# Kernel optimization log

Measured on AMD Instinct MI355X. Metric: run time of the kernel, lower is better.

Reference implementation:

```python
import jax, jax.numpy as jnp
import numpy as np

N_NODES = 100_000
N_EDGES = 1_600_000
HEADS = 3
DIMS = [6, 8, 16, 32]  # in -> conv1 -> conv2 -> conv3 out_feats


def _edge_gat(x, ef, src, dst, W, We, al, ar, ae, b, n_nodes):
    """DGL EdgeGATConv: edge feats modulate attention logits; messages are alpha * W h_src."""
    H, D = al.shape
    ft = (x @ W.T).reshape(n_nodes, H, D)          # [N,H,D] projected node feats
    fe = (ef @ We.T).reshape(-1, H, D)             # [E,H,D] projected edge feats
    el = jnp.sum(ft * al, axis=-1)                 # [N,H]
    er = jnp.sum(ft * ar, axis=-1)                 # [N,H]
    ee = jnp.sum(fe * ae, axis=-1)                 # [E,H]
    e = jax.nn.leaky_relu(el[src] + er[dst] + ee, 0.2)  # [E,H] (DGL default slope 0.2)
    # segment softmax over incoming edges of each dst node
    m = jax.ops.segment_max(e, dst, num_segments=n_nodes)
    m = jnp.where(jnp.isfinite(m), m, 0.0)         # zero-in-degree nodes
    ex = jnp.exp(e - m[dst])
    denom = jax.ops.segment_sum(ex, dst, num_segments=n_nodes)
    a = ex / jnp.maximum(denom[dst], 1e-9)         # [E,H]
    msg = a[:, :, None] * ft[src]                  # [E,H,D]
    out = jax.ops.segment_sum(msg, dst, num_segments=n_nodes)  # [N,H,D]
    return out + b.reshape(1, H, D)


def setup_inputs() -> dict:
    key = jax.random.key(0)
    ks = jax.random.split(key, 32)
    d = {
        "node_feats": jax.random.normal(ks[0], (N_NODES, DIMS[0]), jnp.float32),
        "edge_feats": jax.random.uniform(ks[1], (N_EDGES, 1), jnp.float32),
        "src": jax.random.randint(ks[2], (N_EDGES,), 0, N_NODES, jnp.int32),
        "dst": jax.random.randint(ks[3], (N_EDGES,), 0, N_NODES, jnp.int32),
    }
    ki = 4
    for i in range(3):
        fin, fout = DIMS[i], DIMS[i + 1]
        s = 1.0 / np.sqrt(fin)
        d[f"W{i+1}"] = jax.random.normal(ks[ki], (HEADS * fout, fin), jnp.float32) * s; ki += 1
        d[f"We{i+1}"] = jax.random.normal(ks[ki], (HEADS * fout, 1), jnp.float32); ki += 1
        d[f"al{i+1}"] = jax.random.normal(ks[ki], (HEADS, fout), jnp.float32) * 0.1; ki += 1
        d[f"ar{i+1}"] = jax.random.normal(ks[ki], (HEADS, fout), jnp.float32) * 0.1; ki += 1
        d[f"ae{i+1}"] = jax.random.normal(ks[ki], (HEADS, fout), jnp.float32) * 0.1; ki += 1
        d[f"b{i+1}"] = jnp.zeros((HEADS * fout,), jnp.float32)
    for name, (fo, fi) in [("l1", (16, 32)), ("l2", (4, 16)), ("l3", (1, 4)), ("l4", (1, HEADS))]:
        s = 1.0 / np.sqrt(fi)
        d[name + "w"] = jax.random.uniform(ks[ki], (fo, fi), jnp.float32, -s, s); ki += 1
        d[name + "b"] = jax.random.uniform(ks[ki], (fo,), jnp.float32, -s, s); ki += 1
    return d


def reference(node_feats, edge_feats, src, dst,
              W1, We1, al1, ar1, ae1, b1,
              W2, We2, al2, ar2, ae2, b2,
              W3, We3, al3, ar3, ae3, b3,
              l1w, l1b, l2w, l2b, l3w, l3b, l4w, l4b):
    n = node_feats.shape[0]
    h1 = _edge_gat(node_feats, edge_feats, src, dst, W1, We1, al1, ar1, ae1, b1, n)  # [N,3,8]
    h2 = _edge_gat(h1.mean(axis=1), edge_feats, src, dst, W2, We2, al2, ar2, ae2, b2, n)  # [N,3,16]
    h3 = _edge_gat(h2.mean(axis=1), edge_feats, src, dst, W3, We3, al3, ar3, ae3, b3, n)  # [N,3,32]
    # per-(node,head) MLP head: 32 -> 16 -> 4 -> 1
    x = jax.nn.leaky_relu(h3 @ l1w.T + l1b, 0.01)
    x = jax.nn.leaky_relu(x @ l2w.T + l2b, 0.01)
    x = x @ l3w.T + l3b                            # [N,3,1]
    feats = x.reshape(n, -1) @ l4w.T + l4b         # [N,1] combine heads
    return jnp.max(feats, axis=0)                  # [1]
```

## Files before the change

### kernel.cpp

```cpp
#include <hip/hip_runtime.h>
#include <hip/hip_bf16.h>
#include <hip/hip_fp16.h>

#define HEADS 3

union HU { uint4 u; __half2 h[4]; };

__global__ void prep_ce_kernel(const float* __restrict__ We1, const float* __restrict__ ae1,
                               const float* __restrict__ We2, const float* __restrict__ ae2,
                               const float* __restrict__ We3, const float* __restrict__ ae3,
                               float* __restrict__ ce) {
    int t = threadIdx.x;
    if (t >= 9) return;
    int l = t / 3, h = t % 3;
    const float* We = (l == 0) ? We1 : (l == 1) ? We2 : We3;
    const float* ae = (l == 0) ? ae1 : (l == 1) ? ae2 : ae3;
    int D = (l == 0) ? 8 : (l == 1) ? 16 : 32;
    float s = 0.f;
    for (int d = 0; d < D; d++) s += We[h * D + d] * ae[h * D + d];
    ce[t] = s;
}

__global__ void hist_kernel(const int* __restrict__ dst, int* __restrict__ deg, int E) {
    int tid = blockIdx.x * blockDim.x + threadIdx.x;
    if (tid < E) atomicAdd(&deg[dst[tid]], 1);
}

#define SCAN_BLK 1024
__global__ void scan1_kernel(const int* __restrict__ deg, int* __restrict__ row_ptr,
                             int* __restrict__ partials, int N) {
    __shared__ int sm[SCAN_BLK];
    int t = threadIdx.x;
    int g = blockIdx.x * SCAN_BLK + t;
    int v = (g < N) ? deg[g] : 0;
    sm[t] = v;
    __syncthreads();
    for (int off = 1; off < SCAN_BLK; off <<= 1) {
        int x = (t >= off) ? sm[t - off] : 0;
        __syncthreads();
        sm[t] += x;
        __syncthreads();
    }
    if (g < N) row_ptr[g] = sm[t] - v;
    if (t == SCAN_BLK - 1) partials[blockIdx.x] = sm[t];
}

__global__ void scan2_kernel(int* __restrict__ partials, int NB) {
    __shared__ int sm[128];
    int t = threadIdx.x;
    int v = (t < NB) ? partials[t] : 0;
    sm[t] = v;
    __syncthreads();
    for (int off = 1; off < 128; off <<= 1) {
        int x = (t >= off) ? sm[t - off] : 0;
        __syncthreads();
        sm[t] += x;
        __syncthreads();
    }
    if (t < NB) partials[t] = sm[t] - v;
    if (t == 127) partials[NB] = sm[127];
}

__global__ void scan3_kernel(int* __restrict__ row_ptr, const int* __restrict__ partials,
                             int N, int NB) {
    int g = blockIdx.x * SCAN_BLK + threadIdx.x;
    if (g < N) row_ptr[g] += partials[blockIdx.x];
    if (blockIdx.x == 0 && threadIdx.x == 0) row_ptr[N] = partials[NB];
}

__global__ void scatter_kernel(const int* __restrict__ src, const int* __restrict__ dst,
                               const float* __restrict__ ef, const int* __restrict__ row_ptr,
                               int* __restrict__ cnt, int2* __restrict__ erec, int E) {
    int tid = blockIdx.x * blockDim.x + threadIdx.x;
    if (tid >= E) return;
    int d = dst[tid];
    int pos = row_ptr[d] + atomicAdd(&cnt[d], 1);
    int2 r;
    r.x = src[tid];
    r.y = __float_as_int(ef[tid]);
    erec[pos] = r;
}

template <int FIN, int D, bool MEAN_PREV>
__launch_bounds__(256)
__global__ void node_kernel(const float* __restrict__ xin,
                            const float* __restrict__ W,
                            const float* __restrict__ al,
                            const float* __restrict__ ar,
                            __half* __restrict__ ft,
                            float* __restrict__ el, float* __restrict__ er,
                            int N) {
    int tid = blockIdx.x * blockDim.x + threadIdx.x;
    if (tid >= N * HEADS) return;
    int n = tid / HEADS, h = tid % HEADS;
    float x[FIN];
    if (MEAN_PREV) {
        #pragma unroll
        for (int k = 0; k < FIN; k++)
            x[k] = (xin[(n * HEADS + 0) * FIN + k] +
                    xin[(n * HEADS + 1) * FIN + k] +
                    xin[(n * HEADS + 2) * FIN + k]) * (1.0f / 3.0f);
    } else {
        #pragma unroll
        for (int k = 0; k < FIN; k++) x[k] = xin[n * FIN + k];
    }
    float fv[D];
    float e_l = 0.f, e_r = 0.f;
    #pragma unroll
    for (int d = 0; d < D; d++) {
        const float* wr = &W[(h * D + d) * FIN];
        float f = 0.f;
        #pragma unroll
        for (int k = 0; k < FIN; k++) f += x[k] * wr[k];
        fv[d] = f;
        e_l += f * al[h * D + d];
        e_r += f * ar[h * D + d];
    }
    uint4* dst16 = (uint4*)(ft + (size_t)tid * D);
    #pragma unroll
    for (int q = 0; q < D / 8; q++) {
        HU u;
        #pragma unroll
        for (int j = 0; j < 4; j++)
            u.h[j] = __floats2half2_rn(fv[q * 8 + 2 * j], fv[q * 8 + 2 * j + 1]);
        dst16[q] = u.u;
    }
    el[tid] = e_l;
    er[tid] = e_r;
}

template <int D>
__launch_bounds__(256)
__global__ void agg_kernel(const int* __restrict__ row_ptr, const int2* __restrict__ erec,
                           const __half* __restrict__ ft,
                           const float* __restrict__ el, const float* __restrict__ er,
                           const float* __restrict__ ce,
                           const float* __restrict__ b,
                           float* __restrict__ out,
                           int N) {
    int w = threadIdx.x >> 6;
    int l = threadIdx.x & 63;
    int wl = l / 6;
    int rem = l - wl * 6;
    int s = rem >= 3 ? 1 : 0;
    int h = rem - s * 3;
    int n = (blockIdx.x * 4 + w) * 10 + wl;
    bool active = (wl < 10) && (n < N);

    float m = -3.0e38f, ssum = 0.f;
    float msg[D];
    #pragma unroll
    for (int d = 0; d < D; d++) msg[d] = 0.f;
    int unit = n * HEADS + h;
    float ceh = ce[h];

    if (active) {
        int beg = row_ptr[n], end = row_ptr[n + 1];
        int cnt = end - beg;
        int half = (cnt + 1) >> 1;
        int es = beg + s * half;
        int ee = s ? end : (beg + half);
        float ern = er[unit];

        int e = es;
        for (; e + 3 < ee; e += 4) {
            int2 r0 = erec[e + 0], r1 = erec[e + 1], r2 = erec[e + 2], r3 = erec[e + 3];
            float v0 = el[r0.x * HEADS + h] + ern + __int_as_float(r0.y) * ceh;
            float v1 = el[r1.x * HEADS + h] + ern + __int_as_float(r1.y) * ceh;
            float v2 = el[r2.x * HEADS + h] + ern + __int_as_float(r2.y) * ceh;
            float v3 = el[r3.x * HEADS + h] + ern + __int_as_float(r3.y) * ceh;
            v0 = v0 > 0.f ? v0 : 0.2f * v0;
            v1 = v1 > 0.f ? v1 : 0.2f * v1;
            v2 = v2 > 0.f ? v2 : 0.2f * v2;
            v3 = v3 > 0.f ? v3 : 0.2f * v3;
            float cm = fmaxf(fmaxf(v0, v1), fmaxf(v2, v3));
            if (cm > m) {
                float sc = __expf(m - cm);
                ssum *= sc;
                #pragma unroll
                for (int d = 0; d < D; d++) msg[d] *= sc;
                m = cm;
            }
            float x0 = __expf(v0 - m), x1 = __expf(v1 - m);
            float x2 = __expf(v2 - m), x3 = __expf(v3 - m);
            ssum += (x0 + x1) + (x2 + x3);
            const uint4* f0 = (const uint4*)(ft + ((size_t)r0.x * HEADS + h) * D);
            const uint4* f1 = (const uint4*)(ft + ((size_t)r1.x * HEADS + h) * D);
            const uint4* f2 = (const uint4*)(ft + ((size_t)r2.x * HEADS + h) * D);
            const uint4* f3 = (const uint4*)(ft + ((size_t)r3.x * HEADS + h) * D);
            #pragma unroll
            for (int q = 0; q < D / 8; q++) {
                HU a0, a1, a2, a3;
                a0.u = f0[q]; a1.u = f1[q]; a2.u = f2[q]; a3.u = f3[q];
                #pragma unroll
                for (int j = 0; j < 4; j++) {
                    float2 p0 = __half22float2(a0.h[j]);
                    float2 p1 = __half22float2(a1.h[j]);
                    float2 p2 = __half22float2(a2.h[j]);
                    float2 p3 = __half22float2(a3.h[j]);
                    msg[q * 8 + 2 * j + 0] += x0 * p0.x + x1 * p1.x + x2 * p2.x + x3 * p3.x;
                    msg[q * 8 + 2 * j + 1] += x0 * p0.y + x1 * p1.y + x2 * p2.y + x3 * p3.y;
                }
            }
        }
        for (; e < ee; e++) {
            int2 r = erec[e];
            float v = el[r.x * HEADS + h] + ern + __int_as_float(r.y) * ceh;
            v = v > 0.f ? v : 0.2f * v;
            if (v > m) {
                float sc = __expf(m - v);
                ssum *= sc;
                #pragma unroll
                for (int d = 0; d < D; d++) msg[d] *= sc;
                m = v;
            }
            float x = __expf(v - m);
            ssum += x;
            const uint4* fr = (const uint4*)(ft + ((size_t)r.x * HEADS + h) * D);
            #pragma unroll
            for (int q = 0; q < D / 8; q++) {
                HU a; a.u = fr[q];
                #pragma unroll
                for (int j = 0; j < 4; j++) {
                    float2 p = __half22float2(a.h[j]);
                    msg[q * 8 + 2 * j + 0] += x * p.x;
                    msg[q * 8 + 2 * j + 1] += x * p.y;
                }
            }
        }
    }

    int pl = (s ? (l - 3) : (l + 3)) & 63;
    float om = __shfl(m, pl);
    float osum = __shfl(ssum, pl);
    float M = fmaxf(m, om);
    float sA = __expf(m - M);
    float sB = __expf(om - M);
    float tot = ssum * sA + osum * sB;
    float inv = 1.0f / fmaxf(tot, 1e-9f);
    #pragma unroll
    for (int d = 0; d < D; d++)
        msg[d] = msg[d] * sA + __shfl(msg[d], pl) * sB;

    if (active) {
        int lo = s * (D / 2);
        float* ob = out + (size_t)unit * D + lo;
        #pragma unroll
        for (int d = 0; d < D / 2; d += 4) {
            float4 v;
            v.x = msg[lo + d + 0] * inv + b[h * D + lo + d + 0];
            v.y = msg[lo + d + 1] * inv + b[h * D + lo + d + 1];
            v.z = msg[lo + d + 2] * inv + b[h * D + lo + d + 2];
            v.w = msg[lo + d + 3] * inv + b[h * D + lo + d + 3];
            *(float4*)(ob + d) = v;
        }
    }
}

__global__ void mlp_max_kernel(const float* __restrict__ h3,
                               const float* __restrict__ l1w, const float* __restrict__ l1b,
                               const float* __restrict__ l2w, const float* __restrict__ l2b,
                               const float* __restrict__ l3w, const float* __restrict__ l3b,
                               const float* __restrict__ l4w, const float* __restrict__ l4b,
                               unsigned int* __restrict__ maxkey, int N) {
    int tid = blockIdx.x * blockDim.x + threadIdx.x;
    float feat = -3.0e38f;
    if (tid < N) {
        float acc = l4b[0];
        #pragma unroll
        for (int h = 0; h < HEADS; h++) {
            const float4* vp = (const float4*)&h3[((size_t)tid * HEADS + h) * 32];
            float v[32];
            #pragma unroll
            for (int q = 0; q < 8; q++) {
                float4 t = vp[q];
                v[q * 4 + 0] = t.x; v[q * 4 + 1] = t.y; v[q * 4 + 2] = t.z; v[q * 4 + 3] = t.w;
            }
            float y1[16];
            #pragma unroll
            for (int i = 0; i < 16; i++) {
                float s = l1b[i];
                const float* w = &l1w[i * 32];
                #pragma unroll
                for (int k = 0; k < 32; k++) s += v[k] * w[k];
                y1[i] = s > 0.f ? s : 0.01f * s;
            }
            float y2[4];
            #pragma unroll
            for (int i = 0; i < 4; i++) {
                float s = l2b[i];
                const float* w = &l2w[i * 16];
                #pragma unroll
                for (int k = 0; k < 16; k++) s += y1[k] * w[k];
                y2[i] = s > 0.f ? s : 0.01f * s;
            }
            float y3 = l3b[0];
            #pragma unroll
            for (int k = 0; k < 4; k++) y3 += y2[k] * l3w[k];
            acc += y3 * l4w[h];
        }
        feat = acc;
    }
    #pragma unroll
    for (int off = 32; off > 0; off >>= 1)
        feat = fmaxf(feat, __shfl_down(feat, off));
    if ((threadIdx.x & 63) == 0) {
        unsigned int u = __float_as_uint(feat);
        unsigned int key = (u & 0x80000000u) ? ~u : (u | 0x80000000u);
        atomicMax(maxkey, key);
    }
}

__global__ void finalize_kernel(const unsigned int* __restrict__ maxkey, float* __restrict__ out) {
    unsigned int key = *maxkey;
    unsigned int u = (key & 0x80000000u) ? (key & 0x7FFFFFFFu) : ~key;
    out[0] = __uint_as_float(u);
}

extern "C" void kernel_launch(void* const* d_in, const int* in_sizes, int n_in,
                              void* d_out, int out_size, void* d_ws, size_t ws_size,
                              hipStream_t stream) {
    const float* node_feats = (const float*)d_in[0];
    const float* edge_feats = (const float*)d_in[1];
    const int* src = (const int*)d_in[2];
    const int* dst = (const int*)d_in[3];
    const float* W1  = (const float*)d_in[4];
    const float* We1 = (const float*)d_in[5];
    const float* al1 = (const float*)d_in[6];
    const float* ar1 = (const float*)d_in[7];
    const float* ae1 = (const float*)d_in[8];
    const float* b1  = (const float*)d_in[9];
    const float* W2  = (const float*)d_in[10];
    const float* We2 = (const float*)d_in[11];
    const float* al2 = (const float*)d_in[12];
    const float* ar2 = (const float*)d_in[13];
    const float* ae2 = (const float*)d_in[14];
    const float* b2  = (const float*)d_in[15];
    const float* W3  = (const float*)d_in[16];
    const float* We3 = (const float*)d_in[17];
    const float* al3 = (const float*)d_in[18];
    const float* ar3 = (const float*)d_in[19];
    const float* ae3 = (const float*)d_in[20];
    const float* b3  = (const float*)d_in[21];
    const float* l1w = (const float*)d_in[22];
    const float* l1b = (const float*)d_in[23];
    const float* l2w = (const float*)d_in[24];
    const float* l2b = (const float*)d_in[25];
    const float* l3w = (const float*)d_in[26];
    const float* l3b = (const float*)d_in[27];
    const float* l4w = (const float*)d_in[28];
    const float* l4b = (const float*)d_in[29];

    const int N = in_sizes[0] / 6;
    const int E = in_sizes[2];
    const int NB = (N + SCAN_BLK - 1) / SCAN_BLK;

    char* ws = (char*)d_ws;
    size_t off = 0;
    auto alloc = [&](size_t bytes) -> void* {
        void* p = ws + off;
        off = (off + bytes + 255) & ~(size_t)255;
        return p;
    };
    int* deg            = (int*)alloc((size_t)N * 4);
    int* cnt            = (int*)alloc((size_t)N * 4);
    unsigned int* mkey  = (unsigned int*)alloc(4);
    size_t zero_bytes   = off;
    int* row_ptr        = (int*)alloc((size_t)(N + 1) * 4);
    int* partials       = (int*)alloc((size_t)(NB + 1) * 4);
    int2* erec          = (int2*)alloc((size_t)E * 8);
    __half* ft          = (__half*)alloc((size_t)N * 96 * 2);
    float* outb         = (float*)alloc((size_t)N * 96 * 4);
    float* el           = (float*)alloc((size_t)N * 3 * 4);
    float* er           = (float*)alloc((size_t)N * 3 * 4);
    float* ce           = (float*)alloc(9 * 4);

    hipMemsetAsync(d_ws, 0, zero_bytes, stream);

    prep_ce_kernel<<<1, 16, 0, stream>>>(We1, ae1, We2, ae2, We3, ae3, ce);
    hist_kernel<<<(E + 255) / 256, 256, 0, stream>>>(dst, deg, E);
    scan1_kernel<<<NB, SCAN_BLK, 0, stream>>>(deg, row_ptr, partials, N);
    scan2_kernel<<<1, 128, 0, stream>>>(partials, NB);
    scan3_kernel<<<NB, SCAN_BLK, 0, stream>>>(row_ptr, partials, N, NB);
    scatter_kernel<<<(E + 255) / 256, 256, 0, stream>>>(src, dst, edge_feats, row_ptr, cnt,
                                                        erec, E);

    const int NH = N * HEADS;
    const int gb = (NH + 255) / 256;
    const int gb_agg = (N + 39) / 40;

    node_kernel<6, 8, false><<<gb, 256, 0, stream>>>(node_feats, W1, al1, ar1, ft, el, er, N);
    agg_kernel<8><<<gb_agg, 256, 0, stream>>>(row_ptr, erec, ft, el, er, ce + 0, b1, outb, N);
    node_kernel<8, 16, true><<<gb, 256, 0, stream>>>(outb, W2, al2, ar2, ft, el, er, N);
    agg_kernel<16><<<gb_agg, 256, 0, stream>>>(row_ptr, erec, ft, el, er, ce + 3, b2, outb, N);
    node_kernel<16, 32, true><<<gb, 256, 0, stream>>>(outb, W3, al3, ar3, ft, el, er, N);
    agg_kernel<32><<<gb_agg, 256, 0, stream>>>(row_ptr, erec, ft, el, er, ce + 6, b3, outb, N);

    mlp_max_kernel<<<(N + 255) / 256, 256, 0, stream>>>(outb, l1w, l1b, l2w, l2b, l3w, l3b,
                                                        l4w, l4b, mkey, N);
    finalize_kernel<<<1, 1, 0, stream>>>(mkey, (float*)d_out);
}
```

Before: 520.9 us.

## Build CSR via source-sorted intermediate so per-destination edges are ordered by source

```diff
diff --git a/kernel.cpp b/kernel.cpp
--- a/kernel.cpp
+++ b/kernel.cpp
@@ -21,9 +21,13 @@
     ce[t] = s;
 }
 
-__global__ void hist_kernel(const int* __restrict__ dst, int* __restrict__ deg, int E) {
+__global__ void hist2_kernel(const int* __restrict__ src, const int* __restrict__ dst,
+                             int* __restrict__ sdeg, int* __restrict__ ddeg, int E) {
     int tid = blockIdx.x * blockDim.x + threadIdx.x;
-    if (tid < E) atomicAdd(&deg[dst[tid]], 1);
+    if (tid < E) {
+        atomicAdd(&sdeg[src[tid]], 1);
+        atomicAdd(&ddeg[dst[tid]], 1);
+    }
 }
 
 #define SCAN_BLK 1024
@@ -68,17 +72,23 @@
     if (blockIdx.x == 0 && threadIdx.x == 0) row_ptr[N] = partials[NB];
 }
 
-__global__ void scatter_kernel(const int* __restrict__ src, const int* __restrict__ dst,
-                               const float* __restrict__ ef, const int* __restrict__ row_ptr,
-                               int* __restrict__ cnt, int2* __restrict__ erec, int E) {
+__global__ void scatter_src_kernel(const int* __restrict__ src, const int* __restrict__ dst,
+                                   const float* __restrict__ ef, const int* __restrict__ srow,
+                                   int* __restrict__ scnt, int4* __restrict__ sedge, int E) {
     int tid = blockIdx.x * blockDim.x + threadIdx.x;
     if (tid >= E) return;
-    int d = dst[tid];
-    int pos = row_ptr[d] + atomicAdd(&cnt[d], 1);
-    int2 r;
-    r.x = src[tid];
-    r.y = __float_as_int(ef[tid]);
-    erec[pos] = r;
+    int s = src[tid];
+    int pos = srow[s] + atomicAdd(&scnt[s], 1);
+    sedge[pos] = make_int4(s, dst[tid], __float_as_int(ef[tid]), 0);
+}
+
+__global__ void scatter_dst_kernel(const int4* __restrict__ sedge, const int* __restrict__ drow,
+                                   int* __restrict__ dcnt, int2* __restrict__ erec, int E) {
+    int tid = blockIdx.x * blockDim.x + threadIdx.x;
+    if (tid >= E) return;
+    int4 q = sedge[tid];
+    int pos = drow[q.y] + atomicAdd(&dcnt[q.y], 1);
+    erec[pos] = make_int2(q.x, q.z);
 }
 
 template <int FIN, int D, bool MEAN_PREV>
@@ -156,15 +166,11 @@
 
     if (active) {
         int beg = row_ptr[n], end = row_ptr[n + 1];
-        int cnt = end - beg;
-        int half = (cnt + 1) >> 1;
-        int es = beg + s * half;
-        int ee = s ? end : (beg + half);
         float ern = er[unit];
 
-        int e = es;
-        for (; e + 3 < ee; e += 4) {
-            int2 r0 = erec[e + 0], r1 = erec[e + 1], r2 = erec[e + 2], r3 = erec[e + 3];
+        int e = beg + s;
+        for (; e + 6 < end; e += 8) {
+            int2 r0 = erec[e + 0], r1 = erec[e + 2], r2 = erec[e + 4], r3 = erec[e + 6];
             float v0 = el[r0.x * HEADS + h] + ern + __int_as_float(r0.y) * ceh;
             float v1 = el[r1.x * HEADS + h] + ern + __int_as_float(r1.y) * ceh;
             float v2 = el[r2.x * HEADS + h] + ern + __int_as_float(r2.y) * ceh;
@@ -203,7 +209,7 @@
                 }
             }
         }
-        for (; e < ee; e++) {
+        for (; e < end; e += 2) {
             int2 r = erec[e];
             float v = el[r.x * HEADS + h] + ern + __int_as_float(r.y) * ceh;
             v = v > 0.f ? v : 0.2f * v;
@@ -362,12 +368,16 @@
         off = (off + bytes + 255) & ~(size_t)255;
         return p;
     };
-    int* deg            = (int*)alloc((size_t)N * 4);
-    int* cnt            = (int*)alloc((size_t)N * 4);
+    int* sdeg           = (int*)alloc((size_t)N * 4);
+    int* ddeg           = (int*)alloc((size_t)N * 4);
+    int* scnt           = (int*)alloc((size_t)N * 4);
+    int* dcnt           = (int*)alloc((size_t)N * 4);
     unsigned int* mkey  = (unsigned int*)alloc(4);
     size_t zero_bytes   = off;
-    int* row_ptr        = (int*)alloc((size_t)(N + 1) * 4);
+    int* srow           = (int*)alloc((size_t)(N + 1) * 4);
+    int* drow           = (int*)alloc((size_t)(N + 1) * 4);
     int* partials       = (int*)alloc((size_t)(NB + 1) * 4);
+    int4* sedge         = (int4*)alloc((size_t)E * 16);
     int2* erec          = (int2*)alloc((size_t)E * 8);
     __half* ft          = (__half*)alloc((size_t)N * 96 * 2);
     float* outb         = (float*)alloc((size_t)N * 96 * 4);
@@ -378,23 +388,27 @@
     hipMemsetAsync(d_ws, 0, zero_bytes, stream);
 
     prep_ce_kernel<<<1, 16, 0, stream>>>(We1, ae1, We2, ae2, We3, ae3, ce);
-    hist_kernel<<<(E + 255) / 256, 256, 0, stream>>>(dst, deg, E);
-    scan1_kernel<<<NB, SCAN_BLK, 0, stream>>>(deg, row_ptr, partials, N);
+    hist2_kernel<<<(E + 255) / 256, 256, 0, stream>>>(src, dst, sdeg, ddeg, E);
+    scan1_kernel<<<NB, SCAN_BLK, 0, stream>>>(ddeg, drow, partials, N);
     scan2_kernel<<<1, 128, 0, stream>>>(partials, NB);
-    scan3_kernel<<<NB, SCAN_BLK, 0, stream>>>(row_ptr, partials, N, NB);
-    scatter_kernel<<<(E + 255) / 256, 256, 0, stream>>>(src, dst, edge_feats, row_ptr, cnt,
-                                                        erec, E);
+    scan3_kernel<<<NB, SCAN_BLK, 0, stream>>>(drow, partials, N, NB);
+    scan1_kernel<<<NB, SCAN_BLK, 0, stream>>>(sdeg, srow, partials, N);
+    scan2_kernel<<<1, 128, 0, stream>>>(partials, NB);
+    scan3_kernel<<<NB, SCAN_BLK, 0, stream>>>(srow, partials, N, NB);
+    scatter_src_kernel<<<(E + 255) / 256, 256, 0, stream>>>(src, dst, edge_feats, srow, scnt,
+                                                            sedge, E);
+    scatter_dst_kernel<<<(E + 255) / 256, 256, 0, stream>>>(sedge, drow, dcnt, erec, E);
 
     const int NH = N * HEADS;
     const int gb = (NH + 255) / 256;
     const int gb_agg = (N + 39) / 40;
 
     node_kernel<6, 8, false><<<gb, 256, 0, stream>>>(node_feats, W1, al1, ar1, ft, el, er, N);
-    agg_kernel<8><<<gb_agg, 256, 0, stream>>>(row_ptr, erec, ft, el, er, ce + 0, b1, outb, N);
+    agg_kernel<8><<<gb_agg, 256, 0, stream>>>(drow, erec, ft, el, er, ce + 0, b1, outb, N);
     node_kernel<8, 16, true><<<gb, 256, 0, stream>>>(outb, W2, al2, ar2, ft, el, er, N);
-    agg_kernel<16><<<gb_agg, 256, 0, stream>>>(row_ptr, erec, ft, el, er, ce + 3, b2, outb, N);
+    agg_kernel<16><<<gb_agg, 256, 0, stream>>>(drow, erec, ft, el, er, ce + 3, b2, outb, N);
     node_kernel<16, 32, true><<<gb, 256, 0, stream>>>(outb, W3, al3, ar3, ft, el, er, N);
-    agg_kernel<32><<<gb_agg, 256, 0, stream>>>(row_ptr, erec, ft, el, er, ce + 6, b3, outb, N);
+    agg_kernel<32><<<gb_agg, 256, 0, stream>>>(drow, erec, ft, el, er, ce + 6, b3, outb, N);
 
     mlp_max_kernel<<<(N + 255) / 256, 256, 0, stream>>>(outb, l1w, l1b, l2w, l2b, l3w, l3b,
                                                         l4w, l4b, mkey, N);
```

Measured after the change: 663.1 us. 1.27x slower.

## Sort nodes by degree for balanced aggregation and reuse histogram ranks in scatter

Applied to the files above, without the earlier changes.

```diff
diff --git a/kernel.cpp b/kernel.cpp
--- a/kernel.cpp
+++ b/kernel.cpp
@@ -21,9 +21,10 @@
     ce[t] = s;
 }
 
-__global__ void hist_kernel(const int* __restrict__ dst, int* __restrict__ deg, int E) {
+__global__ void hist_rank_kernel(const int* __restrict__ dst, int* __restrict__ deg,
+                                 int* __restrict__ rank, int E) {
     int tid = blockIdx.x * blockDim.x + threadIdx.x;
-    if (tid < E) atomicAdd(&deg[dst[tid]], 1);
+    if (tid < E) rank[tid] = atomicAdd(&deg[dst[tid]], 1);
 }
 
 #define SCAN_BLK 1024
@@ -70,15 +71,35 @@
 
 __global__ void scatter_kernel(const int* __restrict__ src, const int* __restrict__ dst,
                                const float* __restrict__ ef, const int* __restrict__ row_ptr,
-                               int* __restrict__ cnt, int2* __restrict__ erec, int E) {
+                               const int* __restrict__ rank, int2* __restrict__ erec, int E) {
     int tid = blockIdx.x * blockDim.x + threadIdx.x;
     if (tid >= E) return;
     int d = dst[tid];
-    int pos = row_ptr[d] + atomicAdd(&cnt[d], 1);
+    int pos = row_ptr[d] + rank[tid];
     int2 r;
     r.x = src[tid];
     r.y = __float_as_int(ef[tid]);
     erec[pos] = r;
+}
+
+__global__ void degbin_hist_kernel(const int* __restrict__ deg, int* __restrict__ bins, int N) {
+    int n = blockIdx.x * blockDim.x + threadIdx.x;
+    if (n < N) atomicAdd(&bins[min(deg[n], 63)], 1);
+}
+
+__global__ void degbin_scan_kernel(const int* __restrict__ bins, int* __restrict__ bscan) {
+    if (threadIdx.x == 0) {
+        int run = 0;
+        for (int i = 0; i < 64; i++) { bscan[i] = run; run += bins[i]; }
+    }
+}
+
+__global__ void degbin_scatter_kernel(const int* __restrict__ deg, const int* __restrict__ bscan,
+                                      int* __restrict__ bcnt, int* __restrict__ order, int N) {
+    int n = blockIdx.x * blockDim.x + threadIdx.x;
+    if (n >= N) return;
+    int bin = min(deg[n], 63);
+    order[bscan[bin] + atomicAdd(&bcnt[bin], 1)] = n;
 }
 
 template <int FIN, int D, bool MEAN_PREV>
@@ -132,6 +153,7 @@
 template <int D>
 __launch_bounds__(256)
 __global__ void agg_kernel(const int* __restrict__ row_ptr, const int2* __restrict__ erec,
+                           const int* __restrict__ order,
                            const __half* __restrict__ ft,
                            const float* __restrict__ el, const float* __restrict__ er,
                            const float* __restrict__ ce,
@@ -144,8 +166,10 @@
     int rem = l - wl * 6;
     int s = rem >= 3 ? 1 : 0;
     int h = rem - s * 3;
-    int n = (blockIdx.x * 4 + w) * 10 + wl;
-    bool active = (wl < 10) && (n < N);
+    int slot = (blockIdx.x * 4 + w) * 10 + wl;
+    bool active = (wl < 10) && (slot < N);
+    int n = active ? order[slot] : 0;
+    int blane = l - h;
 
     float m = -3.0e38f, ssum = 0.f;
     float msg[D];
@@ -164,7 +188,15 @@
 
         int e = es;
         for (; e + 3 < ee; e += 4) {
-            int2 r0 = erec[e + 0], r1 = erec[e + 1], r2 = erec[e + 2], r3 = erec[e + 3];
+            int2 r0 = make_int2(0, 0), r1 = r0, r2 = r0, r3 = r0;
+            if (h == 0) {
+                r0 = erec[e + 0]; r1 = erec[e + 1];
+                r2 = erec[e + 2]; r3 = erec[e + 3];
+            }
+            r0.x = __shfl(r0.x, blane); r0.y = __shfl(r0.y, blane);
+            r1.x = __shfl(r1.x, blane); r1.y = __shfl(r1.y, blane);
+            r2.x = __shfl(r2.x, blane); r2.y = __shfl(r2.y, blane);
+            r3.x = __shfl(r3.x, blane); r3.y = __shfl(r3.y, blane);
             float v0 = el[r0.x * HEADS + h] + ern + __int_as_float(r0.y) * ceh;
             float v1 = el[r1.x * HEADS + h] + ern + __int_as_float(r1.y) * ceh;
             float v2 = el[r2.x * HEADS + h] + ern + __int_as_float(r2.y) * ceh;
@@ -363,9 +395,13 @@
         return p;
     };
     int* deg            = (int*)alloc((size_t)N * 4);
-    int* cnt            = (int*)alloc((size_t)N * 4);
+    int* bins           = (int*)alloc(64 * 4);
+    int* bcnt           = (int*)alloc(64 * 4);
     unsigned int* mkey  = (unsigned int*)alloc(4);
     size_t zero_bytes   = off;
+    int* bscan          = (int*)alloc(64 * 4);
+    int* order          = (int*)alloc((size_t)N * 4);
+    int* rank           = (int*)alloc((size_t)E * 4);
     int* row_ptr        = (int*)alloc((size_t)(N + 1) * 4);
     int* partials       = (int*)alloc((size_t)(NB + 1) * 4);
     int2* erec          = (int2*)alloc((size_t)E * 8);
@@ -378,23 +414,26 @@
     hipMemsetAsync(d_ws, 0, zero_bytes, stream);
 
     prep_ce_kernel<<<1, 16, 0, stream>>>(We1, ae1, We2, ae2, We3, ae3, ce);
-    hist_kernel<<<(E + 255) / 256, 256, 0, stream>>>(dst, deg, E);
+    hist_rank_kernel<<<(E + 255) / 256, 256, 0, stream>>>(dst, deg, rank, E);
     scan1_kernel<<<NB, SCAN_BLK, 0, stream>>>(deg, row_ptr, partials, N);
     scan2_kernel<<<1, 128, 0, stream>>>(partials, NB);
     scan3_kernel<<<NB, SCAN_BLK, 0, stream>>>(row_ptr, partials, N, NB);
-    scatter_kernel<<<(E + 255) / 256, 256, 0, stream>>>(src, dst, edge_feats, row_ptr, cnt,
+    scatter_kernel<<<(E + 255) / 256, 256, 0, stream>>>(src, dst, edge_feats, row_ptr, rank,
                                                         erec, E);
+    degbin_hist_kernel<<<(N + 255) / 256, 256, 0, stream>>>(deg, bins, N);
+    degbin_scan_kernel<<<1, 64, 0, stream>>>(bins, bscan);
+    degbin_scatter_kernel<<<(N + 255) / 256, 256, 0, stream>>>(deg, bscan, bcnt, order, N);
 
     const int NH = N * HEADS;
     const int gb = (NH + 255) / 256;
     const int gb_agg = (N + 39) / 40;
 
     node_kernel<6, 8, false><<<gb, 256, 0, stream>>>(node_feats, W1, al1, ar1, ft, el, er, N);
-    agg_kernel<8><<<gb_agg, 256, 0, stream>>>(row_ptr, erec, ft, el, er, ce + 0, b1, outb, N);
+    agg_kernel<8><<<gb_agg, 256, 0, stream>>>(row_ptr, erec, order, ft, el, er, ce + 0, b1, outb, N);
     node_kernel<8, 16, true><<<gb, 256, 0, stream>>>(outb, W2, al2, ar2, ft, el, er, N);
-    agg_kernel<16><<<gb_agg, 256, 0, stream>>>(row_ptr, erec, ft, el, er, ce + 3, b2, outb, N);
+    agg_kernel<16><<<gb_agg, 256, 0, stream>>>(row_ptr, erec, order, ft, el, er, ce + 3, b2, outb, N);
     node_kernel<16, 32, true><<<gb, 256, 0, stream>>>(outb, W3, al3, ar3, ft, el, er, N);
-    agg_kernel<32><<<gb_agg, 256, 0, stream>>>(row_ptr, erec, ft, el, er, ce + 6, b3, outb, N);
+    agg_kernel<32><<<gb_agg, 256, 0, stream>>>(row_ptr, erec, order, ft, el, er, ce + 6, b3, outb, N);
 
     mlp_max_kernel<<<(N + 255) / 256, 256, 0, stream>>>(outb, l1w, l1b, l2w, l2b, l3w, l3b,
                                                         l4w, l4b, mkey, N);
```

Measured after the change: 994.2 us. +90.9%, slower.

## Use head-major node layout and per-head aggregation launches; reuse atomic rank in scatter

Applied to the files above, without the earlier changes.

```diff
diff --git a/kernel.cpp b/kernel.cpp
--- a/kernel.cpp
+++ b/kernel.cpp
@@ -21,9 +21,10 @@
     ce[t] = s;
 }
 
-__global__ void hist_kernel(const int* __restrict__ dst, int* __restrict__ deg, int E) {
+__global__ void hist_rank_kernel(const int* __restrict__ dst, int* __restrict__ deg,
+                                 int* __restrict__ rank, int E) {
     int tid = blockIdx.x * blockDim.x + threadIdx.x;
-    if (tid < E) atomicAdd(&deg[dst[tid]], 1);
+    if (tid < E) rank[tid] = atomicAdd(&deg[dst[tid]], 1);
 }
 
 #define SCAN_BLK 1024
@@ -70,11 +71,11 @@
 
 __global__ void scatter_kernel(const int* __restrict__ src, const int* __restrict__ dst,
                                const float* __restrict__ ef, const int* __restrict__ row_ptr,
-                               int* __restrict__ cnt, int2* __restrict__ erec, int E) {
+                               const int* __restrict__ rank, int2* __restrict__ erec, int E) {
     int tid = blockIdx.x * blockDim.x + threadIdx.x;
     if (tid >= E) return;
     int d = dst[tid];
-    int pos = row_ptr[d] + atomicAdd(&cnt[d], 1);
+    int pos = row_ptr[d] + rank[tid];
     int2 r;
     r.x = src[tid];
     r.y = __float_as_int(ef[tid]);
@@ -92,7 +93,7 @@
                             int N) {
     int tid = blockIdx.x * blockDim.x + threadIdx.x;
     if (tid >= N * HEADS) return;
-    int n = tid / HEADS, h = tid % HEADS;
+    int h = tid / N, n = tid - h * N;
     float x[FIN];
     if (MEAN_PREV) {
         #pragma unroll
@@ -116,7 +117,7 @@
         e_l += f * al[h * D + d];
         e_r += f * ar[h * D + d];
     }
-    uint4* dst16 = (uint4*)(ft + (size_t)tid * D);
+    uint4* dst16 = (uint4*)(ft + ((size_t)h * N + n) * D);
     #pragma unroll
     for (int q = 0; q < D / 8; q++) {
         HU u;
@@ -129,110 +130,100 @@
     er[tid] = e_r;
 }
 
-template <int D>
+template <int D, int EB>
 __launch_bounds__(256)
-__global__ void agg_kernel(const int* __restrict__ row_ptr, const int2* __restrict__ erec,
-                           const __half* __restrict__ ft,
-                           const float* __restrict__ el, const float* __restrict__ er,
-                           const float* __restrict__ ce,
-                           const float* __restrict__ b,
-                           float* __restrict__ out,
-                           int N) {
-    int w = threadIdx.x >> 6;
-    int l = threadIdx.x & 63;
-    int wl = l / 6;
-    int rem = l - wl * 6;
-    int s = rem >= 3 ? 1 : 0;
-    int h = rem - s * 3;
-    int n = (blockIdx.x * 4 + w) * 10 + wl;
-    bool active = (wl < 10) && (n < N);
+__global__ void agg_head_kernel(const int* __restrict__ row_ptr, const int2* __restrict__ erec,
+                                const __half* __restrict__ fth,
+                                const float* __restrict__ elh,
+                                const float* __restrict__ erh,
+                                const float* __restrict__ ce, int h,
+                                const float* __restrict__ b,
+                                float* __restrict__ out,
+                                int N) {
+    int gtid = blockIdx.x * blockDim.x + threadIdx.x;
+    int n = gtid >> 1;
+    if (n >= N) return;
+    int s = gtid & 1;
+    int beg = row_ptr[n], end = row_ptr[n + 1];
+    int cnt = end - beg;
+    int half = (cnt + 1) >> 1;
+    int es = beg + s * half;
+    int ee = s ? end : (beg + half);
+    float ern = erh[n];
+    float ceh = ce[h];
 
     float m = -3.0e38f, ssum = 0.f;
     float msg[D];
     #pragma unroll
     for (int d = 0; d < D; d++) msg[d] = 0.f;
-    int unit = n * HEADS + h;
-    float ceh = ce[h];
-
-    if (active) {
-        int beg = row_ptr[n], end = row_ptr[n + 1];
-        int cnt = end - beg;
-        int half = (cnt + 1) >> 1;
-        int es = beg + s * half;
-        int ee = s ? end : (beg + half);
-        float ern = er[unit];
-
-        int e = es;
-        for (; e + 3 < ee; e += 4) {
-            int2 r0 = erec[e + 0], r1 = erec[e + 1], r2 = erec[e + 2], r3 = erec[e + 3];
-            float v0 = el[r0.x * HEADS + h] + ern + __int_as_float(r0.y) * ceh;
-            float v1 = el[r1.x * HEADS + h] + ern + __int_as_float(r1.y) * ceh;
-            float v2 = el[r2.x * HEADS + h] + ern + __int_as_float(r2.y) * ceh;
-            float v3 = el[r3.x * HEADS + h] + ern + __int_as_float(r3.y) * ceh;
-            v0 = v0 > 0.f ? v0 : 0.2f * v0;
-            v1 = v1 > 0.f ? v1 : 0.2f * v1;
-            v2 = v2 > 0.f ? v2 : 0.2f * v2;
-            v3 = v3 > 0.f ? v3 : 0.2f * v3;
-            float cm = fmaxf(fmaxf(v0, v1), fmaxf(v2, v3));
-            if (cm > m) {
-                float sc = __expf(m - cm);
-                ssum *= sc;
-                #pragma unroll
-                for (int d = 0; d < D; d++) msg[d] *= sc;
-                m = cm;
-            }
-            float x0 = __expf(v0 - m), x1 = __expf(v1 - m);
-            float x2 = __expf(v2 - m), x3 = __expf(v3 - m);
-            ssum += (x0 + x1) + (x2 + x3);
-            const uint4* f0 = (const uint4*)(ft + ((size_t)r0.x * HEADS + h) * D);
-            const uint4* f1 = (const uint4*)(ft + ((size_t)r1.x * HEADS + h) * D);
-            const uint4* f2 = (const uint4*)(ft + ((size_t)r2.x * HEADS + h) * D);
-            const uint4* f3 = (const uint4*)(ft + ((size_t)r3.x * HEADS + h) * D);
-            #pragma unroll
-            for (int q = 0; q < D / 8; q++) {
-                HU a0, a1, a2, a3;
-                a0.u = f0[q]; a1.u = f1[q]; a2.u = f2[q]; a3.u = f3[q];
-                #pragma unroll
-                for (int j = 0; j < 4; j++) {
-                    float2 p0 = __half22float2(a0.h[j]);
-                    float2 p1 = __half22float2(a1.h[j]);
-                    float2 p2 = __half22float2(a2.h[j]);
-                    float2 p3 = __half22float2(a3.h[j]);
-                    msg[q * 8 + 2 * j + 0] += x0 * p0.x + x1 * p1.x + x2 * p2.x + x3 * p3.x;
-                    msg[q * 8 + 2 * j + 1] += x0 * p0.y + x1 * p1.y + x2 * p2.y + x3 * p3.y;
-                }
-            }
-        }
-        for (; e < ee; e++) {
-            int2 r = erec[e];
-            float v = el[r.x * HEADS + h] + ern + __int_as_float(r.y) * ceh;
-            v = v > 0.f ? v : 0.2f * v;
-            if (v > m) {
-                float sc = __expf(m - v);
-                ssum *= sc;
-                #pragma unroll
-                for (int d = 0; d < D; d++) msg[d] *= sc;
-                m = v;
-            }
-            float x = __expf(v - m);
-            ssum += x;
-            const uint4* fr = (const uint4*)(ft + ((size_t)r.x * HEADS + h) * D);
+
+    int e = es;
+    for (; e + EB - 1 < ee; e += EB) {
+        int2 r[EB];
+        #pragma unroll
+        for (int i = 0; i < EB; i++) r[i] = erec[e + i];
+        float v[EB];
+        #pragma unroll
+        for (int i = 0; i < EB; i++) {
+            float t = elh[r[i].x] + ern + __int_as_float(r[i].y) * ceh;
+            v[i] = t > 0.f ? t : 0.2f * t;
+        }
+        float cm = v[0];
+        #pragma unroll
+        for (int i = 1; i < EB; i++) cm = fmaxf(cm, v[i]);
+        if (cm > m) {
+            float sc = __expf(m - cm);
+            ssum *= sc;
+            #pragma unroll
+            for (int d = 0; d < D; d++) msg[d] *= sc;
+            m = cm;
+        }
+        float x[EB];
+        #pragma unroll
+        for (int i = 0; i < EB; i++) { x[i] = __expf(v[i] - m); ssum += x[i]; }
+        #pragma unroll
+        for (int i = 0; i < EB; i++) {
+            const uint4* fr = (const uint4*)(fth + (size_t)r[i].x * D);
             #pragma unroll
             for (int q = 0; q < D / 8; q++) {
                 HU a; a.u = fr[q];
                 #pragma unroll
                 for (int j = 0; j < 4; j++) {
                     float2 p = __half22float2(a.h[j]);
-                    msg[q * 8 + 2 * j + 0] += x * p.x;
-                    msg[q * 8 + 2 * j + 1] += x * p.y;
+                    msg[q * 8 + 2 * j + 0] += x[i] * p.x;
+                    msg[q * 8 + 2 * j + 1] += x[i] * p.y;
                 }
             }
         }
     }
-
-    int pl = (s ? (l - 3) : (l + 3)) & 63;
-    float om = __shfl(m, pl);
-    float osum = __shfl(ssum, pl);
+    for (; e < ee; e++) {
+        int2 r = erec[e];
+        float t = elh[r.x] + ern + __int_as_float(r.y) * ceh;
+        t = t > 0.f ? t : 0.2f * t;
+        if (t > m) {
+            float sc = __expf(m - t);
+            ssum *= sc;
+            #pragma unroll
+            for (int d = 0; d < D; d++) msg[d] *= sc;
+            m = t;
+        }
+        float x = __expf(t - m);
+        ssum += x;
+        const uint4* fr = (const uint4*)(fth + (size_t)r.x * D);
+        #pragma unroll
+        for (int q = 0; q < D / 8; q++) {
+            HU a; a.u = fr[q];
+            #pragma unroll
+            for (int j = 0; j < 4; j++) {
+                float2 p = __half22float2(a.h[j]);
+                msg[q * 8 + 2 * j + 0] += x * p.x;
+                msg[q * 8 + 2 * j + 1] += x * p.y;
+            }
+        }
+    }
+
+    float om = __shfl_xor(m, 1);
+    float osum = __shfl_xor(ssum, 1);
     float M = fmaxf(m, om);
     float sA = __expf(m - M);
     float sB = __expf(om - M);
@@ -240,20 +231,18 @@
     float inv = 1.0f / fmaxf(tot, 1e-9f);
     #pragma unroll
     for (int d = 0; d < D; d++)
-        msg[d] = msg[d] * sA + __shfl(msg[d], pl) * sB;
-
-    if (active) {
-        int lo = s * (D / 2);
-        float* ob = out + (size_t)unit * D + lo;
-        #pragma unroll
-        for (int d = 0; d < D / 2; d += 4) {
-            float4 v;
-            v.x = msg[lo + d + 0] * inv + b[h * D + lo + d + 0];
-            v.y = msg[lo + d + 1] * inv + b[h * D + lo + d + 1];
-            v.z = msg[lo + d + 2] * inv + b[h * D + lo + d + 2];
-            v.w = msg[lo + d + 3] * inv + b[h * D + lo + d + 3];
-            *(float4*)(ob + d) = v;
-        }
+        msg[d] = msg[d] * sA + __shfl_xor(msg[d], 1) * sB;
+
+    int lo = s * (D / 2);
+    float* ob = out + ((size_t)n * HEADS + h) * D + lo;
+    #pragma unroll
+    for (int d = 0; d < D / 2; d += 4) {
+        float4 v;
+        v.x = msg[lo + d + 0] * inv + b[h * D + lo + d + 0];
+        v.y = msg[lo + d + 1] * inv + b[h * D + lo + d + 1];
+        v.z = msg[lo + d + 2] * inv + b[h * D + lo + d + 2];
+        v.w = msg[lo + d + 3] * inv + b[h * D + lo + d + 3];
+        *(float4*)(ob + d) = v;
     }
 }
 
@@ -363,9 +352,9 @@
         return p;
     };
     int* deg            = (int*)alloc((size_t)N * 4);
-    int* cnt            = (int*)alloc((size_t)N * 4);
     unsigned int* mkey  = (unsigned int*)alloc(4);
     size_t zero_bytes   = off;
+    int* rank           = (int*)alloc((size_t)E * 4);
     int* row_ptr        = (int*)alloc((size_t)(N + 1) * 4);
     int* partials       = (int*)alloc((size_t)(NB + 1) * 4);
     int2* erec          = (int2*)alloc((size_t)E * 8);
@@ -378,23 +367,32 @@
     hipMemsetAsync(d_ws, 0, zero_bytes, stream);
 
     prep_ce_kernel<<<1, 16, 0, stream>>>(We1, ae1, We2, ae2, We3, ae3, ce);
-    hist_kernel<<<(E + 255) / 256, 256, 0, stream>>>(dst, deg, E);
+    hist_rank_kernel<<<(E + 255) / 256, 256, 0, stream>>>(dst, deg, rank, E);
     scan1_kernel<<<NB, SCAN_BLK, 0, stream>>>(deg, row_ptr, partials, N);
     scan2_kernel<<<1, 128, 0, stream>>>(partials, NB);
     scan3_kernel<<<NB, SCAN_BLK, 0, stream>>>(row_ptr, partials, N, NB);
-    scatter_kernel<<<(E + 255) / 256, 256, 0, stream>>>(src, dst, edge_feats, row_ptr, cnt,
+    scatter_kernel<<<(E + 255) / 256, 256, 0, stream>>>(src, dst, edge_feats, row_ptr, rank,
                                                         erec, E);
 
     const int NH = N * HEADS;
     const int gb = (NH + 255) / 256;
-    const int gb_agg = (N + 39) / 40;
+    const int gb_agg = (2 * N + 255) / 256;
 
     node_kernel<6, 8, false><<<gb, 256, 0, stream>>>(node_feats, W1, al1, ar1, ft, el, er, N);
-    agg_kernel<8><<<gb_agg, 256, 0, stream>>>(row_ptr, erec, ft, el, er, ce + 0, b1, outb, N);
+    for (int h = 0; h < HEADS; h++)
+        agg_head_kernel<8, 4><<<gb_agg, 256, 0, stream>>>(
+            row_ptr, erec, ft + (size_t)h * N * 8, el + (size_t)h * N, er + (size_t)h * N,
+            ce + 0, h, b1, outb, N);
     node_kernel<8, 16, true><<<gb, 256, 0, stream>>>(outb, W2, al2, ar2, ft, el, er, N);
-    agg_kernel<16><<<gb_agg, 256, 0, stream>>>(row_ptr, erec, ft, el, er, ce + 3, b2, outb, N);
+    for (int h = 0; h < HEADS; h++)
+        agg_head_kernel<16, 4><<<gb_agg, 256, 0, stream>>>(
+            row_ptr, erec, ft + (size_t)h * N * 16, el + (size_t)h * N, er + (size_t)h * N,
+            ce + 3, h, b2, outb, N);
     node_kernel<16, 32, true><<<gb, 256, 0, stream>>>(outb, W3, al3, ar3, ft, el, er, N);
-    agg_kernel<32><<<gb_agg, 256, 0, stream>>>(row_ptr, erec, ft, el, er, ce + 6, b3, outb, N);
+    for (int h = 0; h < HEADS; h++)
+        agg_head_kernel<32, 2><<<gb_agg, 256, 0, stream>>>(
+            row_ptr, erec, ft + (size_t)h * N * 32, el + (size_t)h * N, er + (size_t)h * N,
+            ce + 6, h, b3, outb, N);
 
     mlp_max_kernel<<<(N + 255) / 256, 256, 0, stream>>>(outb, l1w, l1b, l2w, l2b, l3w, l3b,
                                                         l4w, l4b, mkey, N);
```

Result: slower. 533.9 us (+2.5%).
